# Performance work log

Hardware: AMD Instinct MI355X
Metric: run time of the kernel (lower is better)

Reference implementation:

```python
import jax, jax.numpy as jnp
import numpy as np


def setup_inputs() -> dict:
    key = jax.random.key(0)
    k1, k2, k3, k4 = jax.random.split(key, 4)
    B, NEG, S = 16, 128, 128
    D_PRED, D_SAMP, N_PRED = 512, 512, 12
    c = jax.random.normal(k1, (B, S, D_PRED), dtype=jnp.float32)
    z = jax.random.normal(k2, (B, NEG, S, D_SAMP), dtype=jnp.float32)
    # stacked nn.Linear params: W[i] is [out=dimSample, in=dimPrediction]
    W = jax.random.normal(k3, (N_PRED, D_SAMP, D_PRED), dtype=jnp.float32) / np.sqrt(D_PRED)
    b = jax.random.normal(k4, (N_PRED, D_SAMP), dtype=jnp.float32) * 0.01
    return {"c": c, "z": z, "W": W, "b": b, "k": 3}


def reference(c, z, W, b, k):
    # select the k-th predictor Linear: c_proj = c @ W[k]^T + b[k]  -> [B, S, dimSample]
    c_proj = jnp.einsum("bsd,od->bso", c, W[k]) + b[k]
    # (c_proj[:, None] * z).mean(dim=3) expressed as a batched dot product -> [B, Neg, S]
    d_samp = z.shape[-1]
    out = jnp.einsum("bso,bnso->bns", c_proj, z) / d_samp
    return out
```

## Files before the change

### kernel.cpp

```cpp
#include <hip/hip_runtime.h>

#define DIM 512
#define M_ROWS 2048

typedef __attribute__((ext_vector_type(8))) short short8;
typedef __attribute__((ext_vector_type(4))) float f32x4;

static __device__ __forceinline__ short f2bf(float x) {
    unsigned int u = __builtin_bit_cast(unsigned int, x);
    u += 0x7fffu + ((u >> 16) & 1u);
    return (short)(u >> 16);
}

#define K1_PAD 40
__global__ __launch_bounds__(256) void cproj_mfma(
    const float* __restrict__ c, const float* __restrict__ W,
    const float* __restrict__ bias, const int* __restrict__ kptr,
    float* __restrict__ cp) {
    const int ksel = kptr[0];
    const float* __restrict__ Wk = W + (size_t)ksel * DIM * DIM;
    const float* __restrict__ bk = bias + (size_t)ksel * DIM;

    __shared__ short Alds[64][K1_PAD];
    __shared__ short Blds[64][K1_PAD];

    const int bm = blockIdx.x & 31;
    const int bn = blockIdx.x >> 5;
    const int t  = threadIdx.x;
    const int lane = t & 63;
    const int wv   = t >> 6;

    const int srow = t >> 2;
    const int sk   = (t & 3) * 8;

    const float* Ap = c  + (size_t)(bm * 64 + srow) * DIM + sk;
    const float* Bp = Wk + (size_t)(bn * 64 + srow) * DIM + sk;

    float4 a0 = *(const float4*)Ap,       a1 = *(const float4*)(Ap + 4);
    float4 b0 = *(const float4*)Bp,       b1 = *(const float4*)(Bp + 4);

    f32x4 acc[4] = {};

    const int frow = lane & 15;
    const int fk   = (lane >> 4) * 8;

    for (int step = 0; step < 16; ++step) {
        __syncthreads();
        short8 av, bv;
        av[0] = f2bf(a0.x); av[1] = f2bf(a0.y); av[2] = f2bf(a0.z); av[3] = f2bf(a0.w);
        av[4] = f2bf(a1.x); av[5] = f2bf(a1.y); av[6] = f2bf(a1.z); av[7] = f2bf(a1.w);
        bv[0] = f2bf(b0.x); bv[1] = f2bf(b0.y); bv[2] = f2bf(b0.z); bv[3] = f2bf(b0.w);
        bv[4] = f2bf(b1.x); bv[5] = f2bf(b1.y); bv[6] = f2bf(b1.z); bv[7] = f2bf(b1.w);
        *(short8*)&Alds[srow][sk] = av;
        *(short8*)&Blds[srow][sk] = bv;
        __syncthreads();
        if (step < 15) {
            const int off = (step + 1) * 32;
            a0 = *(const float4*)(Ap + off); a1 = *(const float4*)(Ap + off + 4);
            b0 = *(const float4*)(Bp + off); b1 = *(const float4*)(Bp + off + 4);
        }
        const short8 bfrag = *(const short8*)&Blds[wv * 16 + frow][fk];
#pragma unroll
        for (int f = 0; f < 4; ++f) {
            const short8 afrag = *(const short8*)&Alds[f * 16 + frow][fk];
            acc[f] = __builtin_amdgcn_mfma_f32_16x16x32_bf16(afrag, bfrag, acc[f], 0, 0, 0);
        }
    }

    const int col = bn * 64 + wv * 16 + frow;
    const float bias_v = bk[col];
    const int r0 = (lane >> 4) * 4;
#pragma unroll
    for (int f = 0; f < 4; ++f)
#pragma unroll
        for (int r = 0; r < 4; ++r)
            cp[(size_t)(bm * 64 + f * 16 + r0 + r) * DIM + col] = acc[f][r] + bias_v;
}

#define N_STRIDE ((size_t)4 * 128 * 512)
__global__ __launch_bounds__(256) void dot_kernel(
    const float* __restrict__ z, const float* __restrict__ cp,
    float* __restrict__ out) {
    const int bs   = blockIdx.x;
    const int wave = threadIdx.x >> 6;
    const int lane = threadIdx.x & 63;
    const int b = bs >> 7;
    const int s = bs & 127;

    const float* cpr = cp + (size_t)bs * DIM + lane * 8;
    const float4 c0 = *(const float4*)cpr;
    const float4 c1 = *(const float4*)(cpr + 4);

    const float* zp = z + (((size_t)(b * 128 + wave)) * 128 + s) * DIM + lane * 8;
    float4 z0 = *(const float4*)zp;
    float4 z1 = *(const float4*)(zp + 4);

    float* outp = out + ((size_t)b * 128 + wave) * 128 + s;

#pragma unroll 4
    for (int i = 0; i < 32; ++i) {
        const float4 y0 = z0, y1 = z1;
        if (i < 31) {
            zp += N_STRIDE;
            z0 = *(const float4*)zp;
            z1 = *(const float4*)(zp + 4);
        }
        float acc = y0.x * c0.x;
        acc = fmaf(y0.y, c0.y, acc);
        acc = fmaf(y0.z, c0.z, acc);
        acc = fmaf(y0.w, c0.w, acc);
        acc = fmaf(y1.x, c1.x, acc);
        acc = fmaf(y1.y, c1.y, acc);
        acc = fmaf(y1.z, c1.z, acc);
        acc = fmaf(y1.w, c1.w, acc);
#pragma unroll
        for (int off = 32; off; off >>= 1) acc += __shfl_xor(acc, off);
        if (lane == 0) outp[(size_t)i * 4 * 128] = acc * (1.0f / 512.0f);
    }
}

extern "C" void kernel_launch(void* const* d_in, const int* in_sizes, int n_in,
                              void* d_out, int out_size, void* d_ws, size_t ws_size,
                              hipStream_t stream) {
    const float* c    = (const float*)d_in[0];
    const float* z    = (const float*)d_in[1];
    const float* W    = (const float*)d_in[2];
    const float* bias = (const float*)d_in[3];
    const int*   kptr = (const int*)d_in[4];
    float* out = (float*)d_out;
    float* cp  = (float*)d_ws;

    cproj_mfma<<<dim3(256), dim3(256), 0, stream>>>(c, W, bias, kptr, cp);
    dot_kernel<<<dim3(2048), dim3(256), 0, stream>>>(z, cp, out);
}
```

Measured before the change: 123.5 us.

## Remap dot kernel blocks to stream contiguous z rows per (b,n)

```diff
diff --git a/kernel.cpp b/kernel.cpp
--- a/kernel.cpp
+++ b/kernel.cpp
@@ -77,45 +77,66 @@
             cp[(size_t)(bm * 64 + f * 16 + r0 + r) * DIM + col] = acc[f][r] + bias_v;
 }
 
-#define N_STRIDE ((size_t)4 * 128 * 512)
-__global__ __launch_bounds__(256) void dot_kernel(
+#define LD4(p) (*(const float4*)(p))
+__global__ __launch_bounds__(256) void dot_kernel2(
     const float* __restrict__ z, const float* __restrict__ cp,
     float* __restrict__ out) {
-    const int bs   = blockIdx.x;
+    const int j = blockIdx.x;
+    const int r = j >> 3;
+    const int b = ((j & 7) << 1) | (r >> 7);
+    const int n = r & 127;
     const int wave = threadIdx.x >> 6;
     const int lane = threadIdx.x & 63;
-    const int b = bs >> 7;
-    const int s = bs & 127;
 
-    const float* cpr = cp + (size_t)bs * DIM + lane * 8;
-    const float4 c0 = *(const float4*)cpr;
-    const float4 c1 = *(const float4*)(cpr + 4);
+    const float* zp  = z  + (((size_t)(b * 128 + n) * 128 + wave * 2) * DIM) + lane * 8;
+    const float* cpp = cp + (((size_t)b * 128 + wave * 2) * DIM) + lane * 8;
+    float* outp = out + ((size_t)(b * 128 + n)) * 128 + wave * 2;
 
-    const float* zp = z + (((size_t)(b * 128 + wave)) * 128 + s) * DIM + lane * 8;
-    float4 z0 = *(const float4*)zp;
-    float4 z1 = *(const float4*)(zp + 4);
-
-    float* outp = out + ((size_t)b * 128 + wave) * 128 + s;
+    float4 za0 = LD4(zp),         za1 = LD4(zp + 4);
+    float4 zb0 = LD4(zp + DIM),   zb1 = LD4(zp + DIM + 4);
+    float4 ca0 = LD4(cpp),        ca1 = LD4(cpp + 4);
+    float4 cb0 = LD4(cpp + DIM),  cb1 = LD4(cpp + DIM + 4);
 
 #pragma unroll 4
-    for (int i = 0; i < 32; ++i) {
-        const float4 y0 = z0, y1 = z1;
-        if (i < 31) {
-            zp += N_STRIDE;
-            z0 = *(const float4*)zp;
-            z1 = *(const float4*)(zp + 4);
+    for (int i = 0; i < 16; ++i) {
+        const float4 ya0 = za0, ya1 = za1, yb0 = zb0, yb1 = zb1;
+        const float4 da0 = ca0, da1 = ca1, db0 = cb0, db1 = cb1;
+        if (i < 15) {
+            zp  += 8 * DIM;
+            cpp += 8 * DIM;
+            za0 = LD4(zp);        za1 = LD4(zp + 4);
+            zb0 = LD4(zp + DIM);  zb1 = LD4(zp + DIM + 4);
+            ca0 = LD4(cpp);       ca1 = LD4(cpp + 4);
+            cb0 = LD4(cpp + DIM); cb1 = LD4(cpp + DIM + 4);
         }
-        float acc = y0.x * c0.x;
-        acc = fmaf(y0.y, c0.y, acc);
-        acc = fmaf(y0.z, c0.z, acc);
-        acc = fmaf(y0.w, c0.w, acc);
-        acc = fmaf(y1.x, c1.x, acc);
-        acc = fmaf(y1.y, c1.y, acc);
-        acc = fmaf(y1.z, c1.z, acc);
-        acc = fmaf(y1.w, c1.w, acc);
+        float acc0 = ya0.x * da0.x;
+        acc0 = fmaf(ya0.y, da0.y, acc0);
+        acc0 = fmaf(ya0.z, da0.z, acc0);
+        acc0 = fmaf(ya0.w, da0.w, acc0);
+        acc0 = fmaf(ya1.x, da1.x, acc0);
+        acc0 = fmaf(ya1.y, da1.y, acc0);
+        acc0 = fmaf(ya1.z, da1.z, acc0);
+        acc0 = fmaf(ya1.w, da1.w, acc0);
+        float acc1 = yb0.x * db0.x;
+        acc1 = fmaf(yb0.y, db0.y, acc1);
+        acc1 = fmaf(yb0.z, db0.z, acc1);
+        acc1 = fmaf(yb0.w, db0.w, acc1);
+        acc1 = fmaf(yb1.x, db1.x, acc1);
+        acc1 = fmaf(yb1.y, db1.y, acc1);
+        acc1 = fmaf(yb1.z, db1.z, acc1);
+        acc1 = fmaf(yb1.w, db1.w, acc1);
 #pragma unroll
-        for (int off = 32; off; off >>= 1) acc += __shfl_xor(acc, off);
-        if (lane == 0) outp[(size_t)i * 4 * 128] = acc * (1.0f / 512.0f);
+        for (int off = 32; off; off >>= 1) {
+            acc0 += __shfl_xor(acc0, off);
+            acc1 += __shfl_xor(acc1, off);
+        }
+        if (lane == 0) {
+            float2 o2;
+            o2.x = acc0 * (1.0f / 512.0f);
+            o2.y = acc1 * (1.0f / 512.0f);
+            *(float2*)outp = o2;
+        }
+        outp += 8;
     }
 }
 
@@ -131,5 +152,5 @@
     float* cp  = (float*)d_ws;
 
     cproj_mfma<<<dim3(256), dim3(256), 0, stream>>>(c, W, bias, kptr, cp);
-    dot_kernel<<<dim3(2048), dim3(256), 0, stream>>>(z, cp, out);
+    dot_kernel2<<<dim3(2048), dim3(256), 0, stream>>>(z, cp, out);
 }
```

Measured after the change: 133.6 us. 1.08x slower.
